# Optimization experiments

Measured on AMD Instinct MI355X. Metric: run time of the kernel, lower is better.

## Reference

```python
import jax, jax.numpy as jnp
import numpy as np

B, S, D = 4, 2048, 1024


def setup_inputs() -> dict:
    key = jax.random.key(0)
    ks = jax.random.split(key, 9)
    s = 1.0 / np.sqrt(D)
    return {
        "x": jax.random.normal(ks[0], (B, S, D), dtype=jnp.float32),
        "Wq": jax.random.normal(ks[1], (D, D), dtype=jnp.float32) * s,
        "bq": jnp.zeros((D,), dtype=jnp.float32),
        "Wk": jax.random.normal(ks[2], (D, D), dtype=jnp.float32) * s,
        "bk": jnp.zeros((D,), dtype=jnp.float32),
        "Wv": jax.random.normal(ks[3], (D, D), dtype=jnp.float32) * s,
        "bv": jnp.zeros((D,), dtype=jnp.float32),
        "Wo": jax.random.normal(ks[4], (D, D), dtype=jnp.float32) * s,
        "bo": jnp.zeros((D,), dtype=jnp.float32),
    }


def reference(x, Wq, bq, Wk, bk, Wv, bv, Wo, bo):
    # Projections: [B,S,D] @ [D,D] -> [B,S,D]
    q = jnp.einsum("bsd,de->bse", x, Wq) + bq
    k = jnp.einsum("bsd,de->bse", x, Wk) + bk
    v = jnp.einsum("bsd,de->bse", x, Wv) + bv
    # Unscaled single-head attention: scores [B,S,S]
    scores = jnp.einsum("bqd,bkd->bqk", q, k)
    dist = jax.nn.softmax(scores, axis=-1)
    attn = jnp.einsum("bqk,bkd->bqd", dist, v)
    # Output projection + residual
    return jnp.einsum("bsd,de->bse", attn, Wo) + bo + x
```

## Files before the change

### kernel.cpp

```cpp
#include <hip/hip_runtime.h>
#include <hip/hip_bf16.h>

#define DEVI __device__ __forceinline__

typedef __attribute__((ext_vector_type(8))) _Float16 f16x8;
typedef __attribute__((ext_vector_type(4))) float f32x4;
typedef __attribute__((ext_vector_type(4))) unsigned short us4;

DEVI unsigned short f2h(float f) {
  union { _Float16 h; unsigned short u; } v;
  v.h = (_Float16)f;
  return v.u;
}

__global__ void __launch_bounds__(256) k_convert_f16(
    const float* __restrict__ x, unsigned short* __restrict__ o, int n4) {
  int i = blockIdx.x * 256 + threadIdx.x;
  if (i >= n4) return;
  float4 v = reinterpret_cast<const float4*>(x)[i];
  us4 h;
  h[0] = f2h(v.x); h[1] = f2h(v.y); h[2] = f2h(v.z); h[3] = f2h(v.w);
  reinterpret_cast<us4*>(o)[i] = h;
}

__global__ void __launch_bounds__(256) k_transpose4(
    const float* __restrict__ W0, const float* __restrict__ W1,
    const float* __restrict__ W2, const float* __restrict__ W3,
    unsigned short* __restrict__ T0, unsigned short* __restrict__ T1,
    unsigned short* __restrict__ T2, unsigned short* __restrict__ T3, int n) {
  const int zz = blockIdx.z;
  const float* W = (zz == 0) ? W0 : (zz == 1) ? W1 : (zz == 2) ? W2 : W3;
  unsigned short* T = (zz == 0) ? T0 : (zz == 1) ? T1 : (zz == 2) ? T2 : T3;
  __shared__ float t[32][33];
  int tx = threadIdx.x & 31, ty = threadIdx.x >> 5;
  int n0 = blockIdx.x * 32, k0 = blockIdx.y * 32;
#pragma unroll
  for (int r = 0; r < 4; ++r)
    t[ty + r * 8][tx] = W[(size_t)(k0 + ty + r * 8) * n + n0 + tx];
  __syncthreads();
#pragma unroll
  for (int r = 0; r < 4; ++r) {
    int nn = n0 + ty + r * 8;
    T[(size_t)nn * n + k0 + tx] = f2h(t[tx][ty + r * 8]);
  }
}

DEVI void gload16(const unsigned short* gp, unsigned short* lp) {
  __builtin_amdgcn_global_load_lds(
      (const __attribute__((address_space(1))) unsigned int*)gp,
      (__attribute__((address_space(3))) unsigned int*)lp, 16, 0, 0);
}

DEVI void stage_tile64(unsigned short* lbase, const unsigned short* g, int ldg,
                       int wid, int lane) {
#pragma unroll
  for (int it = 0; it < 4; ++it) {
    int chunk = it * 256 + wid * 64 + lane;
    int r = chunk >> 3, s = chunk & 7;
    int c = (s ^ (r & 7)) * 8;
    gload16(g + (size_t)r * ldg + c, lbase + (it * 256 + wid * 64) * 8);
  }
}

DEVI f16x8 frag(const unsigned short* base, int row, int kk, int lr) {
  int slot = (kk * 4 + lr) ^ (row & 7);
  return *reinterpret_cast<const f16x8*>(base + row * 64 + slot * 8);
}

template <int EPI>
__global__ void __launch_bounds__(256, 4) k_gemm(
    const unsigned short* __restrict__ A, const unsigned short* __restrict__ B,
    int K, int ldA, int ldB,
    size_t azs, size_t bzs, size_t czs,
    const float* __restrict__ b0, const float* __restrict__ b1,
    const float* __restrict__ b2, const float* __restrict__ resid,
    float* __restrict__ outF, unsigned short* __restrict__ o0,
    unsigned short* __restrict__ o1, unsigned short* __restrict__ o2, int ldc) {
  __shared__ unsigned short lds[2 * 8192];
  unsigned short* Alds = lds;
  unsigned short* Blds = lds + 8192;

  const int gx = gridDim.x, gy = gridDim.y;
  const int nwg = gx * gy * gridDim.z;
  const int l = (blockIdx.z * gy + blockIdx.y) * gx + blockIdx.x;
  const int nl = (l & 7) * (nwg >> 3) + (l >> 3);
  const int bx = nl % gx;
  const int rem = nl / gx;
  const int by = rem % gy;
  const int z = rem / gy;

  const int tid = threadIdx.x, lane = tid & 63, wid = tid >> 6;
  const int wr = (wid >> 1) * 64, wc = (wid & 1) * 64;
  const int lc = lane & 15, lr = lane >> 4;
  const size_t row0 = (size_t)bx * 128, col0 = (size_t)by * 128;

  const unsigned short* Ag = A + (size_t)z * azs + row0 * ldA;
  const unsigned short* Bg = B + (size_t)z * bzs + col0 * ldB;

  f32x4 acc[4][4] = {};

  for (int k0 = 0; k0 < K; k0 += 64) {
    stage_tile64(Alds, Ag + k0, ldA, wid, lane);
    stage_tile64(Blds, Bg + k0, ldB, wid, lane);
    __syncthreads();
#pragma unroll
    for (int kk = 0; kk < 2; ++kk) {
      f16x8 af[4], bf[4];
#pragma unroll
      for (int i = 0; i < 4; ++i) {
        af[i] = frag(Alds, wr + i * 16 + lc, kk, lr);
        bf[i] = frag(Blds, wc + i * 16 + lc, kk, lr);
      }
#pragma unroll
      for (int mi = 0; mi < 4; ++mi)
#pragma unroll
        for (int ni = 0; ni < 4; ++ni)
          acc[mi][ni] = __builtin_amdgcn_mfma_f32_16x16x32_f16(af[mi], bf[ni], acc[mi][ni], 0, 0, 0);
    }
    __syncthreads();
  }

#pragma unroll
  for (int mi = 0; mi < 4; ++mi) {
#pragma unroll
    for (int ni = 0; ni < 4; ++ni) {
      const int r0 = (int)row0 + wr + mi * 16 + lr * 4;
      const int c = (int)col0 + wc + ni * 16 + lc;
      f32x4 a = acc[mi][ni];
      if (EPI == 0) {
        const int sub = c >> 10;
        const int cc = c & 1023;
        if (sub == 0) {
          float bb = b0[cc];
#pragma unroll
          for (int r = 0; r < 4; ++r)
            o0[(size_t)(r0 + r) * 1024 + cc] = f2h(a[r] + bb);
        } else if (sub == 1) {
          float bb = b1[cc];
#pragma unroll
          for (int r = 0; r < 4; ++r)
            o1[(size_t)(r0 + r) * 1024 + cc] = f2h(a[r] + bb);
        } else {
          float bb = b2[cc];
          us4 pk;
#pragma unroll
          for (int r = 0; r < 4; ++r) pk[r] = f2h(a[r] + bb);
          *reinterpret_cast<us4*>(o2 + ((size_t)(r0 >> 11) * 1024 + cc) * 2048 + (r0 & 2047)) = pk;
        }
      } else if (EPI == 2) {
#pragma unroll
        for (int r = 0; r < 4; ++r)
          outF[(size_t)z * czs + (size_t)(r0 + r) * ldc + c] = a[r];
      } else if (EPI == 3) {
#pragma unroll
        for (int r = 0; r < 4; ++r)
          o0[(size_t)z * czs + (size_t)(r0 + r) * ldc + c] = f2h(a[r]);
      } else {
        float bb = b0[c];
#pragma unroll
        for (int r = 0; r < 4; ++r) {
          size_t idx = (size_t)(r0 + r) * ldc + c;
          outF[idx] = a[r] + bb + resid[idx];
        }
      }
    }
  }
}

__global__ void __launch_bounds__(256) k_softmax(
    const float* __restrict__ S, unsigned short* __restrict__ P) {
  __shared__ float red[4];
  const int row = blockIdx.x, tid = threadIdx.x;
  const int lane = tid & 63, wid = tid >> 6;
  const float* src = S + (size_t)row * 2048;
  float4 v0 = *reinterpret_cast<const float4*>(src + tid * 8);
  float4 v1 = *reinterpret_cast<const float4*>(src + tid * 8 + 4);
  float vv[8] = {v0.x, v0.y, v0.z, v0.w, v1.x, v1.y, v1.z, v1.w};
  float m = vv[0];
#pragma unroll
  for (int j = 1; j < 8; ++j) m = fmaxf(m, vv[j]);
#pragma unroll
  for (int o = 32; o > 0; o >>= 1) m = fmaxf(m, __shfl_xor(m, o));
  if (lane == 0) red[wid] = m;
  __syncthreads();
  m = fmaxf(fmaxf(red[0], red[1]), fmaxf(red[2], red[3]));
  __syncthreads();
  float e[8];
  float s = 0.f;
#pragma unroll
  for (int j = 0; j < 8; ++j) { e[j] = __expf(vv[j] - m); s += e[j]; }
#pragma unroll
  for (int o = 32; o > 0; o >>= 1) s += __shfl_xor(s, o);
  if (lane == 0) red[wid] = s;
  __syncthreads();
  s = red[0] + red[1] + red[2] + red[3];
  float inv = 1.0f / s;
  us4 p0, p1;
#pragma unroll
  for (int j = 0; j < 4; ++j) p0[j] = f2h(e[j] * inv);
#pragma unroll
  for (int j = 0; j < 4; ++j) p1[j] = f2h(e[j + 4] * inv);
  us4* dst = reinterpret_cast<us4*>(P + (size_t)row * 2048 + tid * 8);
  dst[0] = p0;
  dst[1] = p1;
}

extern "C" void kernel_launch(void* const* d_in, const int* in_sizes, int n_in,
                              void* d_out, int out_size, void* d_ws, size_t ws_size,
                              hipStream_t stream) {
  (void)in_sizes; (void)n_in; (void)out_size; (void)ws_size;
  const float* x  = (const float*)d_in[0];
  const float* Wq = (const float*)d_in[1];
  const float* bq = (const float*)d_in[2];
  const float* Wk = (const float*)d_in[3];
  const float* bk = (const float*)d_in[4];
  const float* Wv = (const float*)d_in[5];
  const float* bv = (const float*)d_in[6];
  const float* Wo = (const float*)d_in[7];
  const float* bo = (const float*)d_in[8];
  float* out = (float*)d_out;

  char* p = (char*)d_ws;
  auto take = [&](size_t bytes) {
    char* r = p;
    p += (bytes + 255) & ~(size_t)255;
    return r;
  };
  const size_t SD = (size_t)4 * 2048 * 1024;
  unsigned short* x_h   = (unsigned short*)take(SD * 2);
  unsigned short* q_h   = (unsigned short*)take(SD * 2);
  unsigned short* k_h   = (unsigned short*)take(SD * 2);
  unsigned short* WqkvT = (unsigned short*)take((size_t)3072 * 1024 * 2);
  unsigned short* WoT   = (unsigned short*)take((size_t)1024 * 1024 * 2);
  unsigned short* v_t   = (unsigned short*)take(SD * 2);
  unsigned short* attn  = (unsigned short*)take(SD * 2);
  const size_t SC_B = (size_t)2048 * 2048;
  float* scores       = (float*)take(4 * SC_B * 4);
  unsigned short* Pm  = (unsigned short*)take(4 * SC_B * 2);

  dim3 blk(256);
  k_convert_f16<<<dim3(8192), blk, 0, stream>>>(x, x_h, (int)(SD / 4));
  k_transpose4<<<dim3(32, 32, 4), blk, 0, stream>>>(
      Wq, Wk, Wv, Wo,
      WqkvT, WqkvT + (size_t)1024 * 1024, WqkvT + (size_t)2048 * 1024, WoT, 1024);

  k_gemm<0><<<dim3(64, 24, 1), blk, 0, stream>>>(
      x_h, WqkvT, 1024, 1024, 1024, 0, 0, 0,
      bq, bk, bv, nullptr, nullptr, q_h, k_h, v_t, 0);

  const size_t QZS = (size_t)2048 * 1024;
  const size_t VZS = (size_t)1024 * 2048;
  k_gemm<2><<<dim3(16, 16, 4), blk, 0, stream>>>(
      q_h, k_h, 1024, 1024, 1024, QZS, QZS, SC_B,
      nullptr, nullptr, nullptr, nullptr, scores, nullptr, nullptr, nullptr, 2048);
  k_softmax<<<dim3(8192), blk, 0, stream>>>(scores, Pm);
  k_gemm<3><<<dim3(16, 8, 4), blk, 0, stream>>>(
      Pm, v_t, 2048, 2048, 2048, SC_B, VZS, QZS,
      nullptr, nullptr, nullptr, nullptr, nullptr, attn, nullptr, nullptr, 1024);
  k_gemm<4><<<dim3(64, 8, 1), blk, 0, stream>>>(
      attn, WoT, 1024, 1024, 1024, 0, 0, 0,
      bo, nullptr, nullptr, x, out, nullptr, nullptr, nullptr, 1024);
}
```

Baseline: 233.5 us.

## Write V row-major then transpose separately, swap GEMM grid order, widen convert

The QKV projection now writes V in row-major layout like Q and K, and a new LDS-tiled kernel transposes it into the per-batch layout used by the PV GEMM. This replaces the strided us4 scatter stores in the GEMM epilogue. A template flag swaps the block-to-tile mapping so column tiles vary fastest for the QKV and output-projection GEMMs, which changes which tiles run together and how L2 is reused. The convert kernel handles two float4 per thread with half the blocks. In exchange, the extra transpose adds a launch and one more read and write of V.

```diff
diff --git a/kernel.cpp b/kernel.cpp
--- a/kernel.cpp
+++ b/kernel.cpp
@@ -15,12 +15,17 @@
 
 __global__ void __launch_bounds__(256) k_convert_f16(
     const float* __restrict__ x, unsigned short* __restrict__ o, int n4) {
-  int i = blockIdx.x * 256 + threadIdx.x;
-  if (i >= n4) return;
-  float4 v = reinterpret_cast<const float4*>(x)[i];
-  us4 h;
-  h[0] = f2h(v.x); h[1] = f2h(v.y); h[2] = f2h(v.z); h[3] = f2h(v.w);
-  reinterpret_cast<us4*>(o)[i] = h;
+  int base = blockIdx.x * 512 + threadIdx.x;
+#pragma unroll
+  for (int h = 0; h < 2; ++h) {
+    int i = base + h * 256;
+    if (i < n4) {
+      float4 v = reinterpret_cast<const float4*>(x)[i];
+      us4 u;
+      u[0] = f2h(v.x); u[1] = f2h(v.y); u[2] = f2h(v.z); u[3] = f2h(v.w);
+      reinterpret_cast<us4*>(o)[i] = u;
+    }
+  }
 }
 
 __global__ void __launch_bounds__(256) k_transpose4(
@@ -45,6 +50,36 @@
   }
 }
 
+__global__ void __launch_bounds__(256) k_vtrans(
+    const unsigned short* __restrict__ vr, unsigned short* __restrict__ vt) {
+  __shared__ unsigned short t[64 * 72];
+  const int tid = threadIdx.x;
+  const int s0 = blockIdx.x * 64;
+  const int d0 = blockIdx.y * 64;
+  {
+    const int s = tid >> 2;
+    const int dq = (tid & 3) * 16;
+#pragma unroll
+    for (int c = 0; c < 4; ++c) {
+      us4 v = *reinterpret_cast<const us4*>(vr + (size_t)(s0 + s) * 1024 + d0 + dq + c * 4);
+#pragma unroll
+      for (int e = 0; e < 4; ++e) t[(dq + c * 4 + e) * 72 + s] = v[e];
+    }
+  }
+  __syncthreads();
+  const int lane = tid & 63, wid = tid >> 6;
+  const size_t bofs = (size_t)(s0 >> 11) * 1024 * 2048;
+  const int sloc = (s0 & 2047) + (lane & 15) * 4;
+#pragma unroll
+  for (int i = 0; i < 4; ++i) {
+    const int d = i * 16 + wid * 4 + (lane >> 4);
+    us4 o;
+#pragma unroll
+    for (int j = 0; j < 4; ++j) o[j] = t[d * 72 + (lane & 15) * 4 + j];
+    *reinterpret_cast<us4*>(vt + bofs + (size_t)(d0 + d) * 2048 + sloc) = o;
+  }
+}
+
 DEVI void gload16(const unsigned short* gp, unsigned short* lp) {
   __builtin_amdgcn_global_load_lds(
       (const __attribute__((address_space(1))) unsigned int*)gp,
@@ -67,7 +102,7 @@
   return *reinterpret_cast<const f16x8*>(base + row * 64 + slot * 8);
 }
 
-template <int EPI>
+template <int EPI, int XY>
 __global__ void __launch_bounds__(256, 4) k_gemm(
     const unsigned short* __restrict__ A, const unsigned short* __restrict__ B,
     int K, int ldA, int ldB,
@@ -88,11 +123,13 @@
   const int rem = nl / gx;
   const int by = rem % gy;
   const int z = rem / gy;
+  const int rb = XY ? by : bx;
+  const int cb = XY ? bx : by;
 
   const int tid = threadIdx.x, lane = tid & 63, wid = tid >> 6;
   const int wr = (wid >> 1) * 64, wc = (wid & 1) * 64;
   const int lc = lane & 15, lr = lane >> 4;
-  const size_t row0 = (size_t)bx * 128, col0 = (size_t)by * 128;
+  const size_t row0 = (size_t)rb * 128, col0 = (size_t)cb * 128;
 
   const unsigned short* Ag = A + (size_t)z * azs + row0 * ldA;
   const unsigned short* Bg = B + (size_t)z * bzs + col0 * ldB;
@@ -130,23 +167,11 @@
       if (EPI == 0) {
         const int sub = c >> 10;
         const int cc = c & 1023;
-        if (sub == 0) {
-          float bb = b0[cc];
-#pragma unroll
-          for (int r = 0; r < 4; ++r)
-            o0[(size_t)(r0 + r) * 1024 + cc] = f2h(a[r] + bb);
-        } else if (sub == 1) {
-          float bb = b1[cc];
-#pragma unroll
-          for (int r = 0; r < 4; ++r)
-            o1[(size_t)(r0 + r) * 1024 + cc] = f2h(a[r] + bb);
-        } else {
-          float bb = b2[cc];
-          us4 pk;
-#pragma unroll
-          for (int r = 0; r < 4; ++r) pk[r] = f2h(a[r] + bb);
-          *reinterpret_cast<us4*>(o2 + ((size_t)(r0 >> 11) * 1024 + cc) * 2048 + (r0 & 2047)) = pk;
-        }
+        unsigned short* dst = (sub == 0) ? o0 : (sub == 1) ? o1 : o2;
+        const float bb = ((sub == 0) ? b0 : (sub == 1) ? b1 : b2)[cc];
+#pragma unroll
+        for (int r = 0; r < 4; ++r)
+          dst[(size_t)(r0 + r) * 1024 + cc] = f2h(a[r] + bb);
       } else if (EPI == 2) {
 #pragma unroll
         for (int r = 0; r < 4; ++r)
@@ -230,6 +255,7 @@
   unsigned short* x_h   = (unsigned short*)take(SD * 2);
   unsigned short* q_h   = (unsigned short*)take(SD * 2);
   unsigned short* k_h   = (unsigned short*)take(SD * 2);
+  unsigned short* v_r   = (unsigned short*)take(SD * 2);
   unsigned short* WqkvT = (unsigned short*)take((size_t)3072 * 1024 * 2);
   unsigned short* WoT   = (unsigned short*)take((size_t)1024 * 1024 * 2);
   unsigned short* v_t   = (unsigned short*)take(SD * 2);
@@ -239,25 +265,27 @@
   unsigned short* Pm  = (unsigned short*)take(4 * SC_B * 2);
 
   dim3 blk(256);
-  k_convert_f16<<<dim3(8192), blk, 0, stream>>>(x, x_h, (int)(SD / 4));
+  k_convert_f16<<<dim3(4096), blk, 0, stream>>>(x, x_h, (int)(SD / 4));
   k_transpose4<<<dim3(32, 32, 4), blk, 0, stream>>>(
       Wq, Wk, Wv, Wo,
       WqkvT, WqkvT + (size_t)1024 * 1024, WqkvT + (size_t)2048 * 1024, WoT, 1024);
 
-  k_gemm<0><<<dim3(64, 24, 1), blk, 0, stream>>>(
+  k_gemm<0, 1><<<dim3(24, 64, 1), blk, 0, stream>>>(
       x_h, WqkvT, 1024, 1024, 1024, 0, 0, 0,
-      bq, bk, bv, nullptr, nullptr, q_h, k_h, v_t, 0);
+      bq, bk, bv, nullptr, nullptr, q_h, k_h, v_r, 0);
+
+  k_vtrans<<<dim3(128, 16), blk, 0, stream>>>(v_r, v_t);
 
   const size_t QZS = (size_t)2048 * 1024;
   const size_t VZS = (size_t)1024 * 2048;
-  k_gemm<2><<<dim3(16, 16, 4), blk, 0, stream>>>(
+  k_gemm<2, 0><<<dim3(16, 16, 4), blk, 0, stream>>>(
       q_h, k_h, 1024, 1024, 1024, QZS, QZS, SC_B,
       nullptr, nullptr, nullptr, nullptr, scores, nullptr, nullptr, nullptr, 2048);
   k_softmax<<<dim3(8192), blk, 0, stream>>>(scores, Pm);
-  k_gemm<3><<<dim3(16, 8, 4), blk, 0, stream>>>(
+  k_gemm<3, 0><<<dim3(16, 8, 4), blk, 0, stream>>>(
       Pm, v_t, 2048, 2048, 2048, SC_B, VZS, QZS,
       nullptr, nullptr, nullptr, nullptr, nullptr, attn, nullptr, nullptr, 1024);
-  k_gemm<4><<<dim3(64, 8, 1), blk, 0, stream>>>(
+  k_gemm<4, 1><<<dim3(8, 64, 1), blk, 0, stream>>>(
       attn, WoT, 1024, 1024, 1024, 0, 0, 0,
       bo, nullptr, nullptr, x, out, nullptr, nullptr, nullptr, 1024);
 }
```

Result: faster. 213.2 us (-8.7%).

## Merge prep kernels, 4x4 tile-group swizzle in GEMMs, LDS-staged V transpose epilogue

Applied to the files above, without the earlier changes.

Merges the x conversion and the weight transposes into a single prep launch. Remaps GEMM workgroups so that 4x4 groups of output tiles land next to each other, aiming for better L2 reuse of A and B tiles. The V-projection epilogue now transposes its output through LDS before writing, so global stores are coalesced instead of scattered 4-element writes. The cost is more index arithmetic and extra barriers in the V epilogue.

```diff
diff --git a/kernel.cpp b/kernel.cpp
--- a/kernel.cpp
+++ b/kernel.cpp
@@ -13,35 +13,40 @@
   return v.u;
 }
 
-__global__ void __launch_bounds__(256) k_convert_f16(
-    const float* __restrict__ x, unsigned short* __restrict__ o, int n4) {
-  int i = blockIdx.x * 256 + threadIdx.x;
-  if (i >= n4) return;
-  float4 v = reinterpret_cast<const float4*>(x)[i];
-  us4 h;
-  h[0] = f2h(v.x); h[1] = f2h(v.y); h[2] = f2h(v.z); h[3] = f2h(v.w);
-  reinterpret_cast<us4*>(o)[i] = h;
-}
-
-__global__ void __launch_bounds__(256) k_transpose4(
+__global__ void __launch_bounds__(256) k_prep(
+    const float* __restrict__ x, unsigned short* __restrict__ xh,
     const float* __restrict__ W0, const float* __restrict__ W1,
     const float* __restrict__ W2, const float* __restrict__ W3,
     unsigned short* __restrict__ T0, unsigned short* __restrict__ T1,
-    unsigned short* __restrict__ T2, unsigned short* __restrict__ T3, int n) {
-  const int zz = blockIdx.z;
+    unsigned short* __restrict__ T2, unsigned short* __restrict__ T3) {
+  __shared__ float t[32][33];
+  const int b = blockIdx.x;
+  if (b < 4096) {
+    int base = b * 512 + threadIdx.x;
+#pragma unroll
+    for (int h = 0; h < 2; ++h) {
+      int i = base + h * 256;
+      float4 v = reinterpret_cast<const float4*>(x)[i];
+      us4 u;
+      u[0] = f2h(v.x); u[1] = f2h(v.y); u[2] = f2h(v.z); u[3] = f2h(v.w);
+      reinterpret_cast<us4*>(xh)[i] = u;
+    }
+    return;
+  }
+  const int tt = b - 4096;
+  const int zz = tt >> 10, r = tt & 1023;
+  const int n0 = (r & 31) * 32, k0 = (r >> 5) * 32;
   const float* W = (zz == 0) ? W0 : (zz == 1) ? W1 : (zz == 2) ? W2 : W3;
   unsigned short* T = (zz == 0) ? T0 : (zz == 1) ? T1 : (zz == 2) ? T2 : T3;
-  __shared__ float t[32][33];
   int tx = threadIdx.x & 31, ty = threadIdx.x >> 5;
-  int n0 = blockIdx.x * 32, k0 = blockIdx.y * 32;
-#pragma unroll
-  for (int r = 0; r < 4; ++r)
-    t[ty + r * 8][tx] = W[(size_t)(k0 + ty + r * 8) * n + n0 + tx];
-  __syncthreads();
-#pragma unroll
-  for (int r = 0; r < 4; ++r) {
-    int nn = n0 + ty + r * 8;
-    T[(size_t)nn * n + k0 + tx] = f2h(t[tx][ty + r * 8]);
+#pragma unroll
+  for (int rr = 0; rr < 4; ++rr)
+    t[ty + rr * 8][tx] = W[(size_t)(k0 + ty + rr * 8) * 1024 + n0 + tx];
+  __syncthreads();
+#pragma unroll
+  for (int rr = 0; rr < 4; ++rr) {
+    int nn = n0 + ty + rr * 8;
+    T[(size_t)nn * 1024 + k0 + tx] = f2h(t[tx][ty + rr * 8]);
   }
 }
 
@@ -70,7 +75,7 @@
 template <int EPI>
 __global__ void __launch_bounds__(256, 4) k_gemm(
     const unsigned short* __restrict__ A, const unsigned short* __restrict__ B,
-    int K, int ldA, int ldB,
+    int K, int ldA, int ldB, int TC4,
     size_t azs, size_t bzs, size_t czs,
     const float* __restrict__ b0, const float* __restrict__ b1,
     const float* __restrict__ b2, const float* __restrict__ resid,
@@ -80,19 +85,23 @@
   unsigned short* Alds = lds;
   unsigned short* Blds = lds + 8192;
 
-  const int gx = gridDim.x, gy = gridDim.y;
-  const int nwg = gx * gy * gridDim.z;
-  const int l = (blockIdx.z * gy + blockIdx.y) * gx + blockIdx.x;
+  const int nwg = 16 * gridDim.y * gridDim.z;
+  const int l = (blockIdx.z * gridDim.y + blockIdx.y) * 16 + blockIdx.x;
   const int nl = (l & 7) * (nwg >> 3) + (l >> 3);
-  const int bx = nl % gx;
-  const int rem = nl / gx;
-  const int by = rem % gy;
-  const int z = rem / gy;
+  const int pos = nl & 15;
+  const int st = nl >> 4;
+  const int TR4 = gridDim.y / TC4;
+  const int stc = st % TC4;
+  const int st2 = st / TC4;
+  const int str = st2 % TR4;
+  const int z = st2 / TR4;
+  const int rb = str * 4 + (pos >> 2);
+  const int cb = stc * 4 + (pos & 3);
 
   const int tid = threadIdx.x, lane = tid & 63, wid = tid >> 6;
   const int wr = (wid >> 1) * 64, wc = (wid & 1) * 64;
   const int lc = lane & 15, lr = lane >> 4;
-  const size_t row0 = (size_t)bx * 128, col0 = (size_t)by * 128;
+  const size_t row0 = (size_t)rb * 128, col0 = (size_t)cb * 128;
 
   const unsigned short* Ag = A + (size_t)z * azs + row0 * ldA;
   const unsigned short* Bg = B + (size_t)z * bzs + col0 * ldB;
@@ -118,6 +127,39 @@
           acc[mi][ni] = __builtin_amdgcn_mfma_f32_16x16x32_f16(af[mi], bf[ni], acc[mi][ni], 0, 0, 0);
     }
     __syncthreads();
+  }
+
+  if (EPI == 0 && cb >= 16) {
+    const int dbase = (int)col0 - 2048;
+    unsigned short* vt = lds;
+#pragma unroll
+    for (int h = 0; h < 2; ++h) {
+      __syncthreads();
+      if ((wid >> 1) == h) {
+#pragma unroll
+        for (int mi = 0; mi < 4; ++mi)
+#pragma unroll
+          for (int ni = 0; ni < 4; ++ni) {
+            const int sloc = mi * 16 + lr * 4;
+            const int dloc = wc + ni * 16 + lc;
+            const float bb = b2[dbase + dloc];
+#pragma unroll
+            for (int r = 0; r < 4; ++r)
+              vt[dloc * 68 + sloc + r] = f2h(acc[mi][ni][r] + bb);
+          }
+      }
+      __syncthreads();
+      {
+        const int d = tid >> 1, sc = (tid & 1) * 32;
+        const unsigned short* src = vt + d * 68 + sc;
+        unsigned short* dst = o2 + ((size_t)(row0 >> 11) * 1024 + (dbase + d)) * 2048 +
+                              ((int)(row0 & 2047) + h * 64 + sc);
+#pragma unroll
+        for (int j = 0; j < 8; ++j)
+          reinterpret_cast<us4*>(dst)[j] = *reinterpret_cast<const us4*>(src + j * 4);
+      }
+    }
+    return;
   }
 
 #pragma unroll
@@ -128,25 +170,13 @@
       const int c = (int)col0 + wc + ni * 16 + lc;
       f32x4 a = acc[mi][ni];
       if (EPI == 0) {
-        const int sub = c >> 10;
+        const int sub = cb >> 3;
         const int cc = c & 1023;
-        if (sub == 0) {
-          float bb = b0[cc];
-#pragma unroll
-          for (int r = 0; r < 4; ++r)
-            o0[(size_t)(r0 + r) * 1024 + cc] = f2h(a[r] + bb);
-        } else if (sub == 1) {
-          float bb = b1[cc];
-#pragma unroll
-          for (int r = 0; r < 4; ++r)
-            o1[(size_t)(r0 + r) * 1024 + cc] = f2h(a[r] + bb);
-        } else {
-          float bb = b2[cc];
-          us4 pk;
-#pragma unroll
-          for (int r = 0; r < 4; ++r) pk[r] = f2h(a[r] + bb);
-          *reinterpret_cast<us4*>(o2 + ((size_t)(r0 >> 11) * 1024 + cc) * 2048 + (r0 & 2047)) = pk;
-        }
+        unsigned short* dst = (sub == 0) ? o0 : o1;
+        const float bb = ((sub == 0) ? b0 : b1)[cc];
+#pragma unroll
+        for (int r = 0; r < 4; ++r)
+          dst[(size_t)(r0 + r) * 1024 + cc] = f2h(a[r] + bb);
       } else if (EPI == 2) {
 #pragma unroll
         for (int r = 0; r < 4; ++r)
@@ -239,25 +269,24 @@
   unsigned short* Pm  = (unsigned short*)take(4 * SC_B * 2);
 
   dim3 blk(256);
-  k_convert_f16<<<dim3(8192), blk, 0, stream>>>(x, x_h, (int)(SD / 4));
-  k_transpose4<<<dim3(32, 32, 4), blk, 0, stream>>>(
-      Wq, Wk, Wv, Wo,
-      WqkvT, WqkvT + (size_t)1024 * 1024, WqkvT + (size_t)2048 * 1024, WoT, 1024);
-
-  k_gemm<0><<<dim3(64, 24, 1), blk, 0, stream>>>(
-      x_h, WqkvT, 1024, 1024, 1024, 0, 0, 0,
+  k_prep<<<dim3(8192), blk, 0, stream>>>(
+      x, x_h, Wq, Wk, Wv, Wo,
+      WqkvT, WqkvT + (size_t)1024 * 1024, WqkvT + (size_t)2048 * 1024, WoT);
+
+  k_gemm<0><<<dim3(16, 96, 1), blk, 0, stream>>>(
+      x_h, WqkvT, 1024, 1024, 1024, 6, 0, 0, 0,
       bq, bk, bv, nullptr, nullptr, q_h, k_h, v_t, 0);
 
   const size_t QZS = (size_t)2048 * 1024;
   const size_t VZS = (size_t)1024 * 2048;
   k_gemm<2><<<dim3(16, 16, 4), blk, 0, stream>>>(
-      q_h, k_h, 1024, 1024, 1024, QZS, QZS, SC_B,
+      q_h, k_h, 1024, 1024, 1024, 4, QZS, QZS, SC_B,
       nullptr, nullptr, nullptr, nullptr, scores, nullptr, nullptr, nullptr, 2048);
   k_softmax<<<dim3(8192), blk, 0, stream>>>(scores, Pm);
   k_gemm<3><<<dim3(16, 8, 4), blk, 0, stream>>>(
-      Pm, v_t, 2048, 2048, 2048, SC_B, VZS, QZS,
+      Pm, v_t, 2048, 2048, 2048, 2, SC_B, VZS, QZS,
       nullptr, nullptr, nullptr, nullptr, nullptr, attn, nullptr, nullptr, 1024);
-  k_gemm<4><<<dim3(64, 8, 1), blk, 0, stream>>>(
-      attn, WoT, 1024, 1024, 1024, 0, 0, 0,
+  k_gemm<4><<<dim3(16, 32, 1), blk, 0, stream>>>(
+      attn, WoT, 1024, 1024, 1024, 2, 0, 0, 0,
       bo, nullptr, nullptr, x, out, nullptr, nullptr, nullptr, 1024);
 }
```

Measured after the change: 199.2 us (median of 2 runs). 1.17x faster.
